# Kernel tuning notes

Hardware: AMD Instinct MI355X
Metric: run time of the kernel (lower is better)

Reference implementation:

```python
import jax, jax.numpy as jnp
import numpy as np

N_NODES = 100000
N_PER_GRAPH = 200
N_GRAPHS = N_NODES // N_PER_GRAPH
N_EDGES = 400000
F_IN = 37
H = 128          # node_hidden == transformer_hidden == fc_hidden
HEADS = 8
K_SEEDS = 75     # ceil(0.25 * 300) -> PyG GMT defaults


def _lin(key, out_d, in_d):
    kw, kb = jax.random.split(key)
    w = jax.random.normal(kw, (out_d, in_d), jnp.float32) * float(1.0 / np.sqrt(in_d))
    b = jax.random.normal(kb, (out_d,), jnp.float32) * 0.02
    return w, b


def gcn_layer(x, W, b, src, dst, n):
    # PyG GCNConv with add_self_loops and symmetric deg^-1/2 normalization
    h = x @ W.T                                   # [n, out]
    deg = jnp.ones((n,), h.dtype).at[dst].add(1.0)   # in-degree + self loop
    dinv = jax.lax.rsqrt(deg)
    msg = h[src] * (dinv[src] * dinv[dst])[:, None]  # gather + edge normalize
    agg = jnp.zeros_like(h).at[dst].add(msg)         # scatter-add
    agg = agg + h * (dinv * dinv)[:, None]           # self-loop message
    return agg + b


def attn_block(Q, K, V, fo_W, fo_b):
    # MAB core of GMT: multi-head attention (scaled by sqrt(dim_V)) + rFF residual
    B, nq, d = Q.shape
    dh = d // HEADS
    Qh = Q.reshape(B, nq, HEADS, dh)
    Kh = K.reshape(B, K.shape[1], HEADS, dh)
    Vh = V.reshape(B, V.shape[1], HEADS, dh)
    scores = jnp.einsum('bqhd,bkhd->bhqk', Qh, Kh) / jnp.sqrt(jnp.asarray(d, Q.dtype))
    A = jax.nn.softmax(scores, axis=-1)
    O = jnp.einsum('bhqk,bkhd->bqhd', A, Vh).reshape(B, nq, d)
    out = Q + O
    return out + jax.nn.relu(out @ fo_W.T + fo_b)


def setup_inputs() -> dict:
    key = jax.random.key(0)
    k = iter(jax.random.split(key, 64))
    inp = {}
    inp['herg_em'] = jax.random.normal(next(k), (1, 1280), jnp.float32)
    inp['x'] = jax.random.normal(next(k), (N_NODES, F_IN), jnp.float32)
    inp['edge_attr'] = jax.random.normal(next(k), (N_EDGES, 4), jnp.float32)
    inp['mol_rep'] = jax.random.normal(next(k), (N_GRAPHS, 11), jnp.float32)
    for i, in_d in enumerate([F_IN, H, H, H]):
        inp[f'conv_W{i}'], inp[f'conv_b{i}'] = _lin(next(k), H, in_d)
    inp['lin1_W'], inp['lin1_b'] = _lin(next(k), H, H)
    inp['lin2_W'], inp['lin2_b'] = _lin(next(k), H, H)
    inp['S1'] = jax.random.normal(next(k), (1, K_SEEDS, H), jnp.float32) * 0.1
    for p in ['pma1', 'sab', 'pma2']:
        for nm in ['fq', 'k', 'v', 'fo']:
            inp[f'{p}_{nm}_W'], inp[f'{p}_{nm}_b'] = _lin(next(k), H, H)
    inp['S2'] = jax.random.normal(next(k), (1, 1, H), jnp.float32) * 0.1
    inp['herg_lin_W'], inp['herg_lin_b'] = _lin(next(k), H, 1280)
    inp['herg_out_W'], inp['herg_out_b'] = _lin(next(k), H, 2 * H)
    inp['fc0_W'], inp['fc0_b'] = _lin(next(k), H, H)
    inp['sig_W'], inp['sig_b'] = _lin(next(k), 1, H)
    inp['edge_index'] = jax.random.randint(next(k), (2, N_EDGES), 0, N_NODES, dtype=jnp.int32)
    inp['batch'] = jnp.arange(N_NODES, dtype=jnp.int32) // N_PER_GRAPH
    return inp


def reference(herg_em, x, edge_attr, mol_rep,
              conv_W0, conv_b0, conv_W1, conv_b1, conv_W2, conv_b2, conv_W3, conv_b3,
              lin1_W, lin1_b, lin2_W, lin2_b,
              S1, pma1_fq_W, pma1_fq_b, pma1_k_W, pma1_k_b, pma1_v_W, pma1_v_b, pma1_fo_W, pma1_fo_b,
              sab_fq_W, sab_fq_b, sab_k_W, sab_k_b, sab_v_W, sab_v_b, sab_fo_W, sab_fo_b,
              S2, pma2_fq_W, pma2_fq_b, pma2_k_W, pma2_k_b, pma2_v_W, pma2_v_b, pma2_fo_W, pma2_fo_b,
              herg_lin_W, herg_lin_b, herg_out_W, herg_out_b,
              fc0_W, fc0_b, sig_W, sig_b,
              edge_index, batch):
    src, dst = edge_index[0], edge_index[1]
    n = x.shape[0]

    # stacked GCNConv + ReLU
    h = jax.nn.relu(gcn_layer(x, conv_W0, conv_b0, src, dst, n))
    for W, b in ((conv_W1, conv_b1), (conv_W2, conv_b2), (conv_W3, conv_b3)):
        h = jax.nn.relu(gcn_layer(h, W, b, src, dst, n))

    # GraphMultisetTransformer: lin1 -> GMPool_G -> SelfAtt -> GMPool_I -> lin2
    hx = h @ lin1_W.T + lin1_b                     # [N, H]
    B = N_GRAPHS

    # GMPool_G: seeds attend to GCNConv-projected keys/values (dense per graph)
    Q = jnp.broadcast_to(S1, (B, K_SEEDS, H)) @ pma1_fq_W.T + pma1_fq_b
    K = gcn_layer(hx, pma1_k_W, pma1_k_b, src, dst, n).reshape(B, N_PER_GRAPH, H)
    V = gcn_layer(hx, pma1_v_W, pma1_v_b, src, dst, n).reshape(B, N_PER_GRAPH, H)
    xb = attn_block(Q, K, V, pma1_fo_W, pma1_fo_b)     # [B, 75, H]

    # SelfAtt (SAB)
    Q = xb @ sab_fq_W.T + sab_fq_b
    K = xb @ sab_k_W.T + sab_k_b
    V = xb @ sab_v_W.T + sab_v_b
    xb = attn_block(Q, K, V, sab_fo_W, sab_fo_b)       # [B, 75, H]

    # GMPool_I: single seed, Linear keys/values
    Q = jnp.broadcast_to(S2, (B, 1, H)) @ pma2_fq_W.T + pma2_fq_b
    K = xb @ pma2_k_W.T + pma2_k_b
    V = xb @ pma2_v_W.T + pma2_v_b
    xb = attn_block(Q, K, V, pma2_fo_W, pma2_fo_b)     # [B, 1, H]

    out = xb[:, 0, :] @ lin2_W.T + lin2_b              # [B, H]

    # hERG branch
    herg = jax.nn.relu(herg_em @ herg_lin_W.T + herg_lin_b)   # [1, 128]
    herg = jnp.broadcast_to(herg, (B, herg.shape[1]))
    out = jnp.concatenate([out, herg], axis=1)                 # [B, 256]
    out = jax.nn.relu(out @ herg_out_W.T + herg_out_b)
    out = jax.nn.relu(out @ fc0_W.T + fc0_b)                   # dropout = identity (eval)
    return jax.nn.sigmoid(out @ sig_W.T + sig_b)               # [B, 1]
```

## Files before the change

### kernel.cpp

```cpp
#include <hip/hip_runtime.h>
#include <hip/hip_bf16.h>

typedef unsigned short ushort_t;
typedef unsigned int uint_t;
typedef __attribute__((ext_vector_type(8))) short short8;
typedef __attribute__((ext_vector_type(4))) float float4v;

static constexpr int NN  = 100000;
static constexpr int NE  = 400000;
static constexpr int NB  = 500;
static constexpr int NS  = 75;
static constexpr int H   = 128;
static constexpr float SCALE = 0.08838834764831845f;

union U32 { uint_t u; float f; };
__device__ __forceinline__ float bf2f(ushort_t b){ U32 t; t.u = ((uint_t)b) << 16; return t.f; }
__device__ __forceinline__ ushort_t f2bf(float f){
    U32 t; t.f = f;
    uint_t r = t.u + 0x7fffu + ((t.u >> 16) & 1u);
    return (ushort_t)(r >> 16);
}
__device__ __forceinline__ void fma8(float* a, uint4 u, float c){
    a[0] += c * bf2f((ushort_t)(u.x & 0xffff)); a[1] += c * bf2f((ushort_t)(u.x >> 16));
    a[2] += c * bf2f((ushort_t)(u.y & 0xffff)); a[3] += c * bf2f((ushort_t)(u.y >> 16));
    a[4] += c * bf2f((ushort_t)(u.z & 0xffff)); a[5] += c * bf2f((ushort_t)(u.z >> 16));
    a[6] += c * bf2f((ushort_t)(u.w & 0xffff)); a[7] += c * bf2f((ushort_t)(u.w >> 16));
}

__global__ void k_hist(int* counts, const int* __restrict__ dst, int e){
    int i = blockIdx.x*256 + threadIdx.x;
    if (i < e) atomicAdd(&counts[dst[i]], 1);
}
__global__ __launch_bounds__(256) void k_scan1(const int* __restrict__ counts,
    int* __restrict__ row_start, int* __restrict__ blockSums,
    float* __restrict__ dinv, float* __restrict__ selfc, int n){
    __shared__ int s[256];
    int t = threadIdx.x, i = blockIdx.x*256 + t;
    int v = (i < n) ? counts[i] : 0;
    s[t] = v; __syncthreads();
    #pragma unroll
    for (int off = 1; off < 256; off <<= 1){
        int add = (t >= off) ? s[t-off] : 0;
        __syncthreads();
        s[t] += add;
        __syncthreads();
    }
    if (i < n){
        row_start[i] = s[t] - v;
        float r = rsqrtf(1.f + (float)v);
        dinv[i] = r; selfc[i] = r*r;
    }
    if (t == 255) blockSums[blockIdx.x] = s[255];
}
__global__ __launch_bounds__(512) void k_scan2(const int* __restrict__ blockSums,
    int* __restrict__ blockOff, int nb){
    __shared__ int s[512];
    int t = threadIdx.x;
    int v = (t < nb) ? blockSums[t] : 0;
    s[t] = v; __syncthreads();
    #pragma unroll
    for (int off = 1; off < 512; off <<= 1){
        int add = (t >= off) ? s[t-off] : 0;
        __syncthreads();
        s[t] += add;
        __syncthreads();
    }
    blockOff[t] = s[t] - v;
}
__global__ void k_scan3(int* __restrict__ row_start, int* __restrict__ cursor,
                        const int* __restrict__ blockOff, int n, int total){
    int i = blockIdx.x*256 + threadIdx.x;
    if (i < n){
        int v = row_start[i] + blockOff[i >> 8];
        row_start[i] = v; cursor[i] = v;
    }
    if (i == 0) row_start[n] = total;
}
__global__ void k_fillcsr(const int* __restrict__ src, const int* __restrict__ dst,
    const float* __restrict__ dinv, int* cursor,
    int* __restrict__ srcs_s, float* __restrict__ ce_s, int e){
    int i = blockIdx.x*256 + threadIdx.x;
    if (i < e){
        int d = dst[i], s = src[i];
        int p = atomicAdd(&cursor[d], 1);
        srcs_s[p] = s;
        ce_s[p] = dinv[s] * dinv[d];
    }
}

struct CvtArgs { const float* w[17]; const float* w0; const float* s1; const float* s2; const float* x37; };
static constexpr int CVT_W   = 17*16384;
static constexpr int CVT_W0  = 8192;
static constexpr int CVT_S1  = 9600;
static constexpr int CVT_S2  = 128;
static constexpr int CVT_X   = NN*64;
__global__ void k_cvt_all(CvtArgs a, ushort_t* __restrict__ wbf, ushort_t* __restrict__ w0bf,
                          ushort_t* __restrict__ s1bf, ushort_t* __restrict__ s2bf,
                          ushort_t* __restrict__ xb64, int* __restrict__ counts){
    int i = blockIdx.x*256 + threadIdx.x;
    if (i < NN) counts[i] = 0;
    if (i < CVT_W){ int idx = i >> 14, off = i & 16383; wbf[i] = f2bf(a.w[idx][off]); return; }
    i -= CVT_W;
    if (i < CVT_W0){ int r = i >> 6, c = i & 63; w0bf[i] = (c < 37) ? f2bf(a.w0[r*37 + c]) : (ushort_t)0; return; }
    i -= CVT_W0;
    if (i < CVT_S1){ s1bf[i] = f2bf(a.s1[i]); return; }
    i -= CVT_S1;
    if (i < CVT_S2){ s2bf[i] = f2bf(a.s2[i]); return; }
    i -= CVT_S2;
    if (i < CVT_X){ int r = i >> 6, c = i & 63; xb64[i] = (c < 37) ? f2bf(a.x37[(size_t)r*37 + c]) : (ushort_t)0; return; }
}

__global__ __launch_bounds__(256) void k_seedq(
    const ushort_t* __restrict__ s1bf, const ushort_t* __restrict__ s2bf,
    const ushort_t* __restrict__ W1, const float* __restrict__ bias1,
    const ushort_t* __restrict__ W2q, const float* __restrict__ bias2,
    ushort_t* __restrict__ q0, ushort_t* __restrict__ q2,
    const float* __restrict__ hem, const float* __restrict__ hlW,
    const float* __restrict__ hlb, float* __restrict__ hergv)
{
    int blk = blockIdx.x;
    int tid  = threadIdx.x;
    if (blk == 3){
        __shared__ float e[1280];
        for (int i = tid; i < 1280; i += 256) e[i] = hem[i];
        __syncthreads();
        if (tid < 128){
            float acc = 0.f;
            for (int k = 0; k < 1280; ++k) acc += e[k] * hlW[(size_t)tid*1280 + k];
            hergv[tid] = fmaxf(acc + hlb[tid], 0.f);
        }
        return;
    }
    const ushort_t* x = (blk < 2) ? s1bf : s2bf;
    const ushort_t* W = (blk < 2) ? W1 : W2q;
    const float* bias = (blk < 2) ? bias1 : bias2;
    ushort_t* out = (blk < 2) ? q0 : q2;
    int M = (blk < 2) ? NS : 1;
    int base = (blk < 2) ? blk*64 : 0;
    int wid  = tid >> 6;
    int lane = tid & 63;
    int l15  = lane & 15, quad = lane >> 4;
    int row0 = base + wid*16;
    int ar   = row0 + l15; if (ar > M-1) ar = M-1;
    const short* xr = (const short*)(x + (size_t)ar*H) + quad*8;
    float4v acc[8];
    #pragma unroll
    for (int i = 0; i < 8; ++i) acc[i] = (float4v)0.f;
    #pragma unroll
    for (int kc = 0; kc < 4; ++kc){
        short8 a = *(const short8*)(xr + kc*32);
        #pragma unroll
        for (int nt = 0; nt < 8; ++nt){
            short8 b = *(const short8*)((const short*)(W + (size_t)(nt*16 + l15)*H) + kc*32 + quad*8);
            acc[nt] = __builtin_amdgcn_mfma_f32_16x16x32_bf16(a, b, acc[nt], 0, 0, 0);
        }
    }
    #pragma unroll
    for (int nt = 0; nt < 8; ++nt){
        int c = nt*16 + l15;
        float bv = bias[c];
        #pragma unroll
        for (int reg = 0; reg < 4; ++reg){
            int r = row0 + quad*4 + reg;
            if (r >= M) continue;
            out[(size_t)r*H + c] = f2bf(acc[nt][reg] + bv);
        }
    }
}

template<int NOUT2>
__global__ __launch_bounds__(256, 4) void gemm_fo_then(
    const ushort_t* __restrict__ x, int M,
    const ushort_t* __restrict__ Wfo, const float* __restrict__ bfo,
    const ushort_t* __restrict__ W2,
    const float* __restrict__ b20, const float* __restrict__ b21, const float* __restrict__ b22,
    ushort_t* __restrict__ o0, ushort_t* __restrict__ o1, ushort_t* __restrict__ o2,
    float* __restrict__ o32)
{
    __shared__ ushort_t As[64][136];
    const int tid = threadIdx.x, w = tid >> 6, lane = tid & 63;
    const int l15 = lane & 15, quad = lane >> 4;
    const int row0 = blockIdx.x*64 + w*16;
    int ar = row0 + l15; if (ar > M-1) ar = M-1;
    const short* xr = (const short*)(x + (size_t)ar*H) + quad*8;
    {
        float4v acc[8];
        #pragma unroll
        for (int i = 0; i < 8; ++i) acc[i] = (float4v)0.f;
        #pragma unroll
        for (int kc = 0; kc < 4; ++kc){
            short8 a = *(const short8*)(xr + kc*32);
            #pragma unroll
            for (int nt = 0; nt < 8; ++nt){
                short8 b = *(const short8*)((const short*)(Wfo + (size_t)(nt*16 + l15)*H) + kc*32 + quad*8);
                acc[nt] = __builtin_amdgcn_mfma_f32_16x16x32_bf16(a, b, acc[nt], 0, 0, 0);
            }
        }
        #pragma unroll
        for (int nt = 0; nt < 8; ++nt){
            int c = nt*16 + l15;
            float bv = bfo[c];
            #pragma unroll
            for (int reg = 0; reg < 4; ++reg){
                int r = row0 + quad*4 + reg;
                float v = 0.f;
                if (r < M) v = fmaxf(acc[nt][reg] + bv, 0.f) + bf2f(x[(size_t)r*H + c]);
                As[w*16 + quad*4 + reg][c] = f2bf(v);
            }
        }
    }
    __syncthreads();
    #pragma unroll 1
    for (int n = 0; n < NOUT2; ++n){
        float4v o[8];
        #pragma unroll
        for (int i = 0; i < 8; ++i) o[i] = (float4v)0.f;
        #pragma unroll
        for (int kc = 0; kc < 4; ++kc){
            short8 a = *(const short8*)(&As[w*16 + l15][kc*32 + quad*8]);
            #pragma unroll
            for (int nt = 0; nt < 8; ++nt){
                short8 b = *(const short8*)((const short*)(W2 + (size_t)((n*8 + nt)*16 + l15)*H) + kc*32 + quad*8);
                o[nt] = __builtin_amdgcn_mfma_f32_16x16x32_bf16(a, b, o[nt], 0, 0, 0);
            }
        }
        ushort_t* out = (n == 0) ? o0 : ((n == 1) ? o1 : o2);
        const float* bb = (n == 0) ? b20 : ((n == 1) ? b21 : b22);
        #pragma unroll
        for (int nt = 0; nt < 8; ++nt){
            int c = nt*16 + l15;
            float bv = bb[c];
            #pragma unroll
            for (int reg = 0; reg < 4; ++reg){
                int r = row0 + quad*4 + reg;
                if (r >= M) continue;
                float v = o[nt][reg] + bv;
                if (o32 && n == 0) o32[(size_t)r*H + c] = v;
                else               out[(size_t)r*H + c] = f2bf(v);
            }
        }
    }
}

template<int NOUT, int RELU, int STAGE2, int MINW>
__global__ __launch_bounds__(256, MINW) void k_conv_fused3(
    const ushort_t* __restrict__ x,
    const int* __restrict__ row_st, const int* __restrict__ srcs,
    const float* __restrict__ ces, const float* __restrict__ selfc,
    const ushort_t* __restrict__ W, const float* __restrict__ bias0,
    const float* __restrict__ bias1,
    const ushort_t* __restrict__ W2, const float* __restrict__ bias2,
    ushort_t* __restrict__ out0, ushort_t* __restrict__ out1)
{
    __shared__ ushort_t As[32][136];
    __shared__ ushort_t Bs[(NOUT==16)?32:1][(NOUT==16)?136:1];
    const int tid = threadIdx.x;
    const int node = tid >> 3, qq = tid & 7;
    const int g = blockIdx.x*32 + node;
    float acc[16];
    #pragma unroll
    for (int i = 0; i < 16; ++i) acc[i] = 0.f;
    if (g < NN){
        const uint4* xr = (const uint4*)(x + (size_t)g*H + qq*16);
        float sc = selfc[g];
        uint4 u0 = xr[0], u1 = xr[1];
        fma8(acc+0, u0, sc); fma8(acc+8, u1, sc);
        int e = row_st[g], e1 = row_st[g+1];
        int sA = 0, sB = 0; float cA = 0.f, cB = 0.f;
        if (e < e1){ sA = srcs[e]; cA = ces[e]; }
        if (e + 1 < e1){ sB = srcs[e+1]; cB = ces[e+1]; }
        while (e + 2 <= e1){
            int sA2 = 0, sB2 = 0; float cA2 = 0.f, cB2 = 0.f;
            if (e + 2 < e1){ sA2 = srcs[e+2]; cA2 = ces[e+2]; }
            if (e + 3 < e1){ sB2 = srcs[e+3]; cB2 = ces[e+3]; }
            const uint4* pa = (const uint4*)(x + (size_t)sA*H + qq*16);
            const uint4* pb = (const uint4*)(x + (size_t)sB*H + qq*16);
            uint4 a0 = pa[0], a1 = pa[1];
            uint4 c0 = pb[0], c1 = pb[1];
            fma8(acc+0, a0, cA); fma8(acc+8, a1, cA);
            fma8(acc+0, c0, cB); fma8(acc+8, c1, cB);
            sA = sA2; sB = sB2; cA = cA2; cB = cB2;
            e += 2;
        }
        if (e < e1){
            const uint4* pa = (const uint4*)(x + (size_t)sA*H + qq*16);
            uint4 a0 = pa[0], a1 = pa[1];
            fma8(acc+0, a0, cA); fma8(acc+8, a1, cA);
        }
    }
    {
        uint_t* dst = (uint_t*)&As[node][qq*16];
        #pragma unroll
        for (int i = 0; i < 8; ++i)
            dst[i] = (uint_t)f2bf(acc[2*i]) | ((uint_t)f2bf(acc[2*i+1]) << 16);
    }
    __syncthreads();
    const int w = tid >> 6, lane = tid & 63, l15 = lane & 15, quad = lane >> 4;
    const int rt = w & 1;
    constexpr int NT = NOUT/2;
    const int ct0 = (w >> 1) * NT;
    float4v o[NT];
    #pragma unroll
    for (int t = 0; t < NT; ++t) o[t] = (float4v)0.f;
    #pragma unroll
    for (int kc = 0; kc < 4; ++kc){
        short8 a = *(const short8*)(&As[rt*16 + l15][kc*32 + quad*8]);
        #pragma unroll
        for (int t = 0; t < NT; ++t){
            short8 bfr = *(const short8*)(W + (size_t)((ct0 + t)*16 + l15)*H + kc*32 + quad*8);
            o[t] = __builtin_amdgcn_mfma_f32_16x16x32_bf16(a, bfr, o[t], 0, 0, 0);
        }
    }
    __syncthreads();
    #pragma unroll
    for (int t = 0; t < NT; ++t){
        int cg = (ct0 + t)*16 + l15;
        #pragma unroll
        for (int r = 0; r < 4; ++r){
            float v;
            if (NOUT == 8 || cg < 128){
                v = o[t][r] + bias0[cg];
                if (RELU) v = fmaxf(v, 0.f);
                As[rt*16 + quad*4 + r][cg] = f2bf(v);
            } else {
                v = o[t][r] + bias1[cg - 128];
                if (RELU) v = fmaxf(v, 0.f);
                Bs[rt*16 + quad*4 + r][cg - 128] = f2bf(v);
            }
        }
    }
    __syncthreads();
    if (STAGE2){
        float4v o2[4];
        #pragma unroll
        for (int t = 0; t < 4; ++t) o2[t] = (float4v)0.f;
        const int ct2 = (w >> 1) * 4;
        #pragma unroll
        for (int kc = 0; kc < 4; ++kc){
            short8 a = *(const short8*)(&As[rt*16 + l15][kc*32 + quad*8]);
            #pragma unroll
            for (int t = 0; t < 4; ++t){
                short8 bfr = *(const short8*)(W2 + (size_t)((ct2 + t)*16 + l15)*H + kc*32 + quad*8);
                o2[t] = __builtin_amdgcn_mfma_f32_16x16x32_bf16(a, bfr, o2[t], 0, 0, 0);
            }
        }
        __syncthreads();
        #pragma unroll
        for (int t = 0; t < 4; ++t){
            int cg = (ct2 + t)*16 + l15;
            #pragma unroll
            for (int r = 0; r < 4; ++r)
                As[rt*16 + quad*4 + r][cg] = f2bf(o2[t][r] + bias2[cg]);
        }
        __syncthreads();
    }
    if (g < NN){
        if (NOUT == 16){
            size_t kb = ((size_t)(qq >> 1)*NN + (size_t)g)*32 + (size_t)(qq & 1)*16;
            ((uint4*)(out0 + kb))[0] = *(const uint4*)&As[node][qq*16];
            ((uint4*)(out0 + kb))[1] = *(const uint4*)&As[node][qq*16 + 8];
            ((uint4*)(out1 + kb))[0] = *(const uint4*)&Bs[node][qq*16];
            ((uint4*)(out1 + kb))[1] = *(const uint4*)&Bs[node][qq*16 + 8];
        } else {
            uint4* op = (uint4*)(out0 + (size_t)g*H + qq*16);
            const uint4* sp = (const uint4*)&As[node][qq*16];
            op[0] = sp[0]; op[1] = sp[1];
        }
    }
}

__global__ __launch_bounds__(256, 8) void k_conv0b(
    const ushort_t* __restrict__ x,
    const int* __restrict__ row_st, const int* __restrict__ srcs,
    const float* __restrict__ ces, const float* __restrict__ selfc,
    const ushort_t* __restrict__ W,
    const float* __restrict__ bias,
    ushort_t* __restrict__ out)
{
    __shared__ ushort_t As[32][136];
    const int tid = threadIdx.x;
    const int node = tid >> 3, qq = tid & 7;
    const int g = blockIdx.x*32 + node;
    float acc[8];
    #pragma unroll
    for (int i = 0; i < 8; ++i) acc[i] = 0.f;
    if (g < NN){
        const uint4* xr = (const uint4*)(x + (size_t)g*64 + qq*8);
        float sc = selfc[g];
        fma8(acc, xr[0], sc);
        int e = row_st[g], e1 = row_st[g+1];
        int sA = 0, sB = 0; float cA = 0.f, cB = 0.f;
        if (e < e1){ sA = srcs[e]; cA = ces[e]; }
        if (e + 1 < e1){ sB = srcs[e+1]; cB = ces[e+1]; }
        while (e + 2 <= e1){
            int sA2 = 0, sB2 = 0; float cA2 = 0.f, cB2 = 0.f;
            if (e + 2 < e1){ sA2 = srcs[e+2]; cA2 = ces[e+2]; }
            if (e + 3 < e1){ sB2 = srcs[e+3]; cB2 = ces[e+3]; }
            uint4 a0 = *(const uint4*)(x + (size_t)sA*64 + qq*8);
            uint4 c0 = *(const uint4*)(x + (size_t)sB*64 + qq*8);
            fma8(acc, a0, cA);
            fma8(acc, c0, cB);
            sA = sA2; sB = sB2; cA = cA2; cB = cB2;
            e += 2;
        }
        if (e < e1){
            uint4 a0 = *(const uint4*)(x + (size_t)sA*64 + qq*8);
            fma8(acc, a0, cA);
        }
    }
    {
        uint_t* dst = (uint_t*)&As[node][qq*8];
        #pragma unroll
        for (int i = 0; i < 4; ++i)
            dst[i] = (uint_t)f2bf(acc[2*i]) | ((uint_t)f2bf(acc[2*i+1]) << 16);
    }
    __syncthreads();
    const int w = tid >> 6, lane = tid & 63, l15 = lane & 15, quad = lane >> 4;
    const int rt = w & 1;
    const int ct0 = (w >> 1) * 4;
    float4v o[4];
    #pragma unroll
    for (int t = 0; t < 4; ++t) o[t] = (float4v)0.f;
    #pragma unroll
    for (int kc = 0; kc < 2; ++kc){
        short8 a = *(const short8*)(&As[rt*16 + l15][kc*32 + quad*8]);
        #pragma unroll
        for (int t = 0; t < 4; ++t){
            short8 bfr = *(const short8*)(W + (size_t)((ct0 + t)*16 + l15)*64 + kc*32 + quad*8);
            o[t] = __builtin_amdgcn_mfma_f32_16x16x32_bf16(a, bfr, o[t], 0, 0, 0);
        }
    }
    __syncthreads();
    #pragma unroll
    for (int t = 0; t < 4; ++t){
        int cg = (ct0 + t)*16 + l15;
        #pragma unroll
        for (int r = 0; r < 4; ++r)
            As[rt*16 + quad*4 + r][cg] = f2bf(fmaxf(o[t][r] + bias[cg], 0.f));
    }
    __syncthreads();
    if (g < NN){
        uint4* op = (uint4*)(out + (size_t)g*H + qq*16);
        const uint4* sp = (const uint4*)&As[node][qq*16];
        op[0] = sp[0]; op[1] = sp[1];
    }
}

template<int NK, int HM>
__global__ __launch_bounds__(256) void k_attn_mfma(
    const ushort_t* __restrict__ Q, int qbs,
    const ushort_t* __restrict__ K, const ushort_t* __restrict__ V,
    ushort_t* __restrict__ out, int nq)
{
    constexpr int NKT = (NK + 15) / 16;
    constexpr int NKC = (NK + 31) / 32;
    __shared__ ushort_t Ks[2][208][24];
    __shared__ ushort_t Vs[2][16][232];
    __shared__ ushort_t Ps[4][16][232];
    int b = blockIdx.x >> 2, hp = blockIdx.x & 3;
    int h0 = hp*2;
    int tid = threadIdx.x;
    {
        uint_t* p = (uint_t*)&Ps[0][0][0];
        for (int i = tid; i < 4*16*232/2; i += 256) p[i] = 0;
    }
    const ushort_t* Kb = HM ? (K + ((size_t)hp*NB + b)*NK*32)
                            : (K + (size_t)b*NK*H + h0*16);
    for (int idx = tid; idx < NK*8; idx += 256){
        int key = idx >> 3, p = idx & 7;
        int hh = p >> 2, dl = (p & 3)*4;
        const uint_t* src = HM ? (const uint_t*)(Kb + (size_t)key*32 + hh*16 + dl)
                               : (const uint_t*)(Kb + (size_t)key*H + hh*16 + dl);
        uint_t* d = (uint_t*)&Ks[hh][key][dl];
        d[0] = src[0]; d[1] = src[1];
    }
    const ushort_t* Vb = HM ? (V + ((size_t)hp*NB + b)*NK*32)
                            : (V + (size_t)b*NK*H + h0*16);
    for (int idx = tid; idx < NK*8; idx += 256){
        int key = idx >> 3, p = idx & 7;
        int hh = p >> 2, dl = (p & 3)*4;
        const ushort_t* src = HM ? (Vb + (size_t)key*32 + hh*16 + dl)
                                 : (Vb + (size_t)key*H + hh*16 + dl);
        Vs[hh][dl+0][key] = src[0];
        Vs[hh][dl+1][key] = src[1];
        Vs[hh][dl+2][key] = src[2];
        Vs[hh][dl+3][key] = src[3];
    }
    for (int idx = tid; idx < 2*16*(232-NK); idx += 256){
        int key = NK + idx % (232-NK), r = idx / (232-NK);
        Vs[r>>4][r&15][key] = 0;
    }
    __syncthreads();

    int w = tid >> 6, lane = tid & 63;
    int hh = w >> 1, half = w & 1;
    int h = h0 + hh;
    int l15 = lane & 15, quad = lane >> 4;
    bool klow = (quad < 2);
    int nqt = (nq + 15) >> 4;
    int split = (nqt + 1) >> 1;
    int qt0 = half ? split : 0;
    int qt1 = half ? nqt : split;
    for (int qt = qt0; qt < qt1; ++qt){
        int qr = qt*16 + l15; if (qr > nq-1) qr = nq-1;
        short8 av = *(const short8*)(Q + (size_t)b*qbs + (size_t)qr*H + h*16 + (quad & 1)*8);
        short8 zero8 = (short8)0;
        short8 afrag = klow ? av : zero8;
        float4v s[NKT];
        #pragma unroll
        for (int kt = 0; kt < NKT; ++kt){
            short8 bv = *(const short8*)(&Ks[hh][kt*16 + l15][(quad & 1)*8]);
            short8 bfrag = klow ? bv : zero8;
            s[kt] = __builtin_amdgcn_mfma_f32_16x16x32_bf16(afrag, bfrag, (float4v)0.f, 0, 0, 0);
        }
        float mx[4] = {-1e30f, -1e30f, -1e30f, -1e30f};
        #pragma unroll
        for (int kt = 0; kt < NKT; ++kt){
            if (kt*16 + l15 >= NK){ s[kt][0]=-1e30f; s[kt][1]=-1e30f; s[kt][2]=-1e30f; s[kt][3]=-1e30f; }
            #pragma unroll
            for (int r = 0; r < 4; ++r) mx[r] = fmaxf(mx[r], s[kt][r]);
        }
        #pragma unroll
        for (int off = 1; off < 16; off <<= 1){
            #pragma unroll
            for (int r = 0; r < 4; ++r) mx[r] = fmaxf(mx[r], __shfl_xor(mx[r], off));
        }
        float sum[4] = {0.f, 0.f, 0.f, 0.f};
        #pragma unroll
        for (int kt = 0; kt < NKT; ++kt){
            #pragma unroll
            for (int r = 0; r < 4; ++r){
                float e = __expf((s[kt][r] - mx[r]) * SCALE);
                sum[r] += e;
                Ps[w][quad*4 + r][kt*16 + l15] = f2bf(e);
            }
        }
        #pragma unroll
        for (int off = 1; off < 16; off <<= 1){
            #pragma unroll
            for (int r = 0; r < 4; ++r) sum[r] += __shfl_xor(sum[r], off);
        }
        float4v o = (float4v)0.f;
        #pragma unroll
        for (int kc = 0; kc < NKC; ++kc){
            short8 pa = *(const short8*)(&Ps[w][l15][kc*32 + quad*8]);
            short8 vb = *(const short8*)(&Vs[hh][l15][kc*32 + quad*8]);
            o = __builtin_amdgcn_mfma_f32_16x16x32_bf16(pa, vb, o, 0, 0, 0);
        }
        #pragma unroll
        for (int r = 0; r < 4; ++r){
            int row = qt*16 + quad*4 + r;
            if (row < nq){
                float qv = bf2f(Q[(size_t)b*qbs + (size_t)row*H + h*16 + l15]);
                out[((size_t)b*nq + row)*H + h*16 + l15] = f2bf(qv + o[r] / sum[r]);
            }
        }
    }
}

__global__ __launch_bounds__(256) void k_pma2_final(
    const ushort_t* __restrict__ q2,
    const ushort_t* __restrict__ K,
    const ushort_t* __restrict__ V,
    const ushort_t* __restrict__ p2foW,
    const float* __restrict__ p2fob,
    const ushort_t* __restrict__ lin2W,
    const float* __restrict__ lin2b,
    const float* __restrict__ hergv,
    const float* __restrict__ hoW, const float* __restrict__ hob,
    const float* __restrict__ fcW, const float* __restrict__ fcb,
    const float* __restrict__ sW,  const float* __restrict__ sb,
    float* __restrict__ outp)
{
    int b = blockIdx.x, t = threadIdx.x;
    __shared__ float sc[8][76];
    __shared__ float sumh[8];
    __shared__ ushort_t xa[128];
    __shared__ ushort_t xb3[128];
    __shared__ float tt[128];
    __shared__ float v256[256];
    __shared__ float red[128];

    const ushort_t* Kb = K + (size_t)b*NS*H;
    const ushort_t* Vb = V + (size_t)b*NS*H;

    {
        int h = t >> 5, l32 = t & 31;
        const ushort_t* qr = q2 + h*16;
        for (int k = l32; k < NS; k += 32){
            const ushort_t* kr = Kb + (size_t)k*H + h*16;
            float s = 0.f;
            #pragma unroll
            for (int d = 0; d < 16; ++d) s += bf2f(qr[d]) * bf2f(kr[d]);
            sc[h][k] = s;
        }
    }
    __syncthreads();
    if (t < 128){
        int hh = t >> 4, i = t & 15;
        float mx = -1e30f;
        for (int k = i; k < NS; k += 16) mx = fmaxf(mx, sc[hh][k]);
        #pragma unroll
        for (int off = 1; off < 16; off <<= 1) mx = fmaxf(mx, __shfl_xor(mx, off));
        float sm = 0.f;
        for (int k = i; k < NS; k += 16){
            float e = __expf((sc[hh][k] - mx) * SCALE);
            sc[hh][k] = e;
            sm += e;
        }
        #pragma unroll
        for (int off = 1; off < 16; off <<= 1) sm += __shfl_xor(sm, off);
        if (i == 0) sumh[hh] = sm;
    }
    __syncthreads();
    if (t < 128){
        int hh = t >> 4;
        float o = 0.f;
        for (int k = 0; k < NS; ++k) o += sc[hh][k] * bf2f(Vb[(size_t)k*H + t]);
        xa[t] = f2bf(bf2f(q2[t]) + o / sumh[hh]);
    }
    __syncthreads();
    if (t < 128){
        float a = 0.f;
        const ushort_t* wr = p2foW + (size_t)t*H;
        for (int k = 0; k < H; ++k) a += bf2f(xa[k]) * bf2f(wr[k]);
        xb3[t] = f2bf(fmaxf(a + p2fob[t], 0.f) + bf2f(xa[t]));
    }
    __syncthreads();
    if (t < 128){
        float a = 0.f;
        const ushort_t* wr = lin2W + (size_t)t*H;
        for (int k = 0; k < H; ++k) a += bf2f(xb3[k]) * bf2f(wr[k]);
        v256[t] = a + lin2b[t];
        v256[128 + t] = hergv[t];
    }
    __syncthreads();
    if (t < 128){
        float acc = 0.f;
        const float* wr = hoW + (size_t)t*256;
        for (int k = 0; k < 256; ++k) acc += v256[k] * wr[k];
        tt[t] = fmaxf(acc + hob[t], 0.f);
    }
    __syncthreads();
    if (t < 128){
        float acc = 0.f;
        const float* wr = fcW + (size_t)t*128;
        for (int k = 0; k < 128; ++k) acc += tt[k] * wr[k];
        float uv = fmaxf(acc + fcb[t], 0.f);
        red[t] = uv * sW[t];
    }
    __syncthreads();
    for (int s = 64; s > 0; s >>= 1){
        if (t < s) red[t] += red[t + s];
        __syncthreads();
    }
    if (t == 0){
        float logit = red[0] + sb[0];
        outp[b] = 1.f / (1.f + expf(-logit));
    }
}

extern "C" void kernel_launch(void* const* d_in, const int* in_sizes, int n_in,
                              void* d_out, int out_size, void* d_ws, size_t ws_size,
                              hipStream_t stream)
{
    (void)in_sizes; (void)n_in; (void)out_size; (void)ws_size;
    const float* herg_em = (const float*)d_in[0];
    const float* x_in    = (const float*)d_in[1];
    const float* convW[4] = {(const float*)d_in[4], (const float*)d_in[6], (const float*)d_in[8], (const float*)d_in[10]};
    const float* convB[4] = {(const float*)d_in[5], (const float*)d_in[7], (const float*)d_in[9], (const float*)d_in[11]};
    const float* lin1W = (const float*)d_in[12]; const float* lin1b = (const float*)d_in[13];
    const float* lin2W = (const float*)d_in[14]; const float* lin2b = (const float*)d_in[15];
    const float* S1    = (const float*)d_in[16];
    const float* p1fqW = (const float*)d_in[17]; const float* p1fqb = (const float*)d_in[18];
    const float* p1kW  = (const float*)d_in[19]; const float* p1kb  = (const float*)d_in[20];
    const float* p1vW  = (const float*)d_in[21]; const float* p1vb  = (const float*)d_in[22];
    const float* p1foW = (const float*)d_in[23]; const float* p1fob = (const float*)d_in[24];
    const float* sfqW  = (const float*)d_in[25]; const float* sfqb  = (const float*)d_in[26];
    const float* skW   = (const float*)d_in[27]; const float* skb   = (const float*)d_in[28];
    const float* svW   = (const float*)d_in[29]; const float* svb   = (const float*)d_in[30];
    const float* sfoW  = (const float*)d_in[31]; const float* sfob  = (const float*)d_in[32];
    const float* p2fqW = (const float*)d_in[33]; const float* p2fqb = (const float*)d_in[34];
    const float* p2kW  = (const float*)d_in[35]; const float* p2kb  = (const float*)d_in[36];
    const float* p2vW  = (const float*)d_in[37]; const float* p2vb  = (const float*)d_in[38];
    const float* p2foW = (const float*)d_in[39]; const float* p2fob = (const float*)d_in[40];
    const float* S2    = (const float*)d_in[41];
    const float* hlW   = (const float*)d_in[42]; const float* hlb   = (const float*)d_in[43];
    const float* hoW   = (const float*)d_in[44]; const float* hob   = (const float*)d_in[45];
    const float* fcW   = (const float*)d_in[46]; const float* fcb   = (const float*)d_in[47];
    const float* sW    = (const float*)d_in[48]; const float* sb    = (const float*)d_in[49];
    const int*  ei    = (const int*)d_in[50];
    const int*  esrc  = ei;
    const int*  edst  = ei + NE;
    float* outp = (float*)d_out;

    char* WS = (char*)d_ws;
    int*   counts = (int*)(WS + 0);
    int*   cursor = (int*)(WS + 400384);
    int*   row_st = (int*)(WS + 800768);
    int*   bSums  = (int*)(WS + 1201152);
    int*   bOff   = (int*)(WS + 1203200);
    float* dinv   = (float*)(WS + 1205248);
    float* selfc  = (float*)(WS + 1605632);
    int*   srcs_s = (int*)(WS + 2005632);
    float* ce_s   = (float*)(WS + 3605632);
    ushort_t* wbf = (ushort_t*)(WS + 5205632);
    ushort_t* w0bf= (ushort_t*)(WS + 5762688);
    ushort_t* s1bf= (ushort_t*)(WS + 5779072);
    ushort_t* s2bf= (ushort_t*)(WS + 5798272);
    ushort_t* q0  = (ushort_t*)(WS + 5798528);
    ushort_t* q2  = (ushort_t*)(WS + 5817728);
    float* hergv  = (float*)(WS + 5817984);
    ushort_t* xb64= (ushort_t*)(WS + 6074496);
    ushort_t* b0  = (ushort_t*)(WS + 18874496);
    ushort_t* b1  = (ushort_t*)(WS + 44474496);
    ushort_t* b2  = (ushort_t*)(WS + 70074496);
    ushort_t* xA  = (ushort_t*)(WS + 95674496);
    ushort_t* xB  = (ushort_t*)(WS + 105275520);
    ushort_t* xQ  = (ushort_t*)(WS + 114876544);
    ushort_t* xK  = (ushort_t*)(WS + 124477568);
    ushort_t* xV  = (ushort_t*)(WS + 134078592);

    const int gN   = (NN + 255)/256;
    const int gE   = (NE + 255)/256;
    const int gC   = (NN + 31)/32;
    const int gXb  = (NB*NS + 63)/64;

    CvtArgs ca;
    ca.w[0]=convW[1]; ca.w[1]=convW[2]; ca.w[2]=convW[3]; ca.w[3]=lin1W; ca.w[4]=lin2W;
    ca.w[5]=p1kW; ca.w[6]=p1vW; ca.w[7]=p1foW;
    ca.w[8]=sfqW; ca.w[9]=skW; ca.w[10]=svW; ca.w[11]=sfoW;
    ca.w[12]=p2kW; ca.w[13]=p2vW; ca.w[14]=p2foW; ca.w[15]=p1fqW; ca.w[16]=p2fqW;
    ca.w0 = convW[0]; ca.s1 = S1; ca.s2 = S2; ca.x37 = x_in;
    const int cvtTotal = CVT_W + CVT_W0 + CVT_S1 + CVT_S2 + CVT_X;
    k_cvt_all<<<(cvtTotal + 255)/256, 256, 0, stream>>>(ca, wbf, w0bf, s1bf, s2bf, xb64, counts);

    k_hist  <<<gE, 256, 0, stream>>>(counts, edst, NE);
    k_scan1 <<<gN, 256, 0, stream>>>(counts, row_st, bSums, dinv, selfc, NN);
    k_scan2 <<<1, 512, 0, stream>>>(bSums, bOff, gN);
    k_scan3 <<<gN, 256, 0, stream>>>(row_st, cursor, bOff, NN, NE);
    k_fillcsr<<<gE, 256, 0, stream>>>(esrc, edst, dinv, cursor, srcs_s, ce_s, NE);

    k_seedq<<<4, 256, 0, stream>>>(s1bf, s2bf, wbf + (size_t)15*16384, p1fqb,
                                   wbf + (size_t)16*16384, p2fqb, q0, q2,
                                   herg_em, hlW, hlb, hergv);

    k_conv0b<<<gC, 256, 0, stream>>>(xb64, row_st, srcs_s, ce_s, selfc, w0bf, convB[0], b0);
    k_conv_fused3<8,1,0,8><<<gC, 256, 0, stream>>>(b0, row_st, srcs_s, ce_s, selfc,
        wbf + (size_t)0*16384, convB[1], nullptr, nullptr, nullptr, b1, nullptr);
    k_conv_fused3<8,1,0,8><<<gC, 256, 0, stream>>>(b1, row_st, srcs_s, ce_s, selfc,
        wbf + (size_t)1*16384, convB[2], nullptr, nullptr, nullptr, b0, nullptr);
    k_conv_fused3<8,1,1,8><<<gC, 256, 0, stream>>>(b0, row_st, srcs_s, ce_s, selfc,
        wbf + (size_t)2*16384, convB[3], nullptr, wbf + (size_t)3*16384, lin1b, b1, nullptr);
    k_conv_fused3<16,0,0,4><<<gC, 256, 0, stream>>>(b1, row_st, srcs_s, ce_s, selfc,
        wbf + (size_t)5*16384, p1kb, p1vb, nullptr, nullptr, b2, b0);
    k_attn_mfma<200,1><<<NB*4, 256, 0, stream>>>(q0, 0, b2, b0, xA, NS);
    gemm_fo_then<3><<<gXb, 256, 0, stream>>>(xA, NB*NS, wbf + (size_t)7*16384, p1fob,
        wbf + (size_t)8*16384, sfqb, skb, svb, xQ, xK, xV, nullptr);
    k_attn_mfma<75,0><<<NB*4, 256, 0, stream>>>(xQ, NS*H, xK, xV, xB, NS);
    gemm_fo_then<2><<<gXb, 256, 0, stream>>>(xB, NB*NS, wbf + (size_t)11*16384, sfob,
        wbf + (size_t)12*16384, p2kb, p2vb, nullptr, xK, xV, nullptr, nullptr);
    k_pma2_final<<<NB, 256, 0, stream>>>(q2, xK, xV,
        wbf + (size_t)14*16384, p2fob, wbf + (size_t)4*16384, lin2b,
        hergv, hoW, hob, fcW, fcb, sW, sb, outp);
}
```

Baseline: 771.9 us.

## Fuse post-PMA1 tail into one per-graph kernel kept in shared memory

Replaces the two gemm_fo_then launches, the SAB attention launch and the final PMA2 kernel with one kernel, one block per graph. All intermediate Q/K/V and activations for a graph's 75 seeds stay in LDS instead of round-tripping through global memory. The intent is to remove roughly 4 launches and several tens of MB of intermediate traffic. In exchange it uses large LDS per block, so at most one or two blocks fit per CU, and there are only 500 blocks, which may leave the GPU underutilized and serialize the GEMM work within each block.

Measured after the change: 731.7 us. -5.2%, faster.

```diff
diff --git a/kernel.cpp b/kernel.cpp
--- a/kernel.cpp
+++ b/kernel.cpp
@@ -164,80 +164,6 @@
             int r = row0 + quad*4 + reg;
             if (r >= M) continue;
             out[(size_t)r*H + c] = f2bf(acc[nt][reg] + bv);
-        }
-    }
-}
-
-template<int NOUT2>
-__global__ __launch_bounds__(256, 4) void gemm_fo_then(
-    const ushort_t* __restrict__ x, int M,
-    const ushort_t* __restrict__ Wfo, const float* __restrict__ bfo,
-    const ushort_t* __restrict__ W2,
-    const float* __restrict__ b20, const float* __restrict__ b21, const float* __restrict__ b22,
-    ushort_t* __restrict__ o0, ushort_t* __restrict__ o1, ushort_t* __restrict__ o2,
-    float* __restrict__ o32)
-{
-    __shared__ ushort_t As[64][136];
-    const int tid = threadIdx.x, w = tid >> 6, lane = tid & 63;
-    const int l15 = lane & 15, quad = lane >> 4;
-    const int row0 = blockIdx.x*64 + w*16;
-    int ar = row0 + l15; if (ar > M-1) ar = M-1;
-    const short* xr = (const short*)(x + (size_t)ar*H) + quad*8;
-    {
-        float4v acc[8];
-        #pragma unroll
-        for (int i = 0; i < 8; ++i) acc[i] = (float4v)0.f;
-        #pragma unroll
-        for (int kc = 0; kc < 4; ++kc){
-            short8 a = *(const short8*)(xr + kc*32);
-            #pragma unroll
-            for (int nt = 0; nt < 8; ++nt){
-                short8 b = *(const short8*)((const short*)(Wfo + (size_t)(nt*16 + l15)*H) + kc*32 + quad*8);
-                acc[nt] = __builtin_amdgcn_mfma_f32_16x16x32_bf16(a, b, acc[nt], 0, 0, 0);
-            }
-        }
-        #pragma unroll
-        for (int nt = 0; nt < 8; ++nt){
-            int c = nt*16 + l15;
-            float bv = bfo[c];
-            #pragma unroll
-            for (int reg = 0; reg < 4; ++reg){
-                int r = row0 + quad*4 + reg;
-                float v = 0.f;
-                if (r < M) v = fmaxf(acc[nt][reg] + bv, 0.f) + bf2f(x[(size_t)r*H + c]);
-                As[w*16 + quad*4 + reg][c] = f2bf(v);
-            }
-        }
-    }
-    __syncthreads();
-    #pragma unroll 1
-    for (int n = 0; n < NOUT2; ++n){
-        float4v o[8];
-        #pragma unroll
-        for (int i = 0; i < 8; ++i) o[i] = (float4v)0.f;
-        #pragma unroll
-        for (int kc = 0; kc < 4; ++kc){
-            short8 a = *(const short8*)(&As[w*16 + l15][kc*32 + quad*8]);
-            #pragma unroll
-            for (int nt = 0; nt < 8; ++nt){
-                short8 b = *(const short8*)((const short*)(W2 + (size_t)((n*8 + nt)*16 + l15)*H) + kc*32 + quad*8);
-                o[nt] = __builtin_amdgcn_mfma_f32_16x16x32_bf16(a, b, o[nt], 0, 0, 0);
-            }
-        }
-        ushort_t* out = (n == 0) ? o0 : ((n == 1) ? o1 : o2);
-        const float* bb = (n == 0) ? b20 : ((n == 1) ? b21 : b22);
-        #pragma unroll
-        for (int nt = 0; nt < 8; ++nt){
-            int c = nt*16 + l15;
-            float bv = bb[c];
-            #pragma unroll
-            for (int reg = 0; reg < 4; ++reg){
-                int r = row0 + quad*4 + reg;
-                if (r >= M) continue;
-                float v = o[nt][reg] + bv;
-                if (o32 && n == 0) o32[(size_t)r*H + c] = v;
-                else               out[(size_t)r*H + c] = f2bf(v);
-            }
         }
     }
 }
@@ -558,105 +484,301 @@
     }
 }
 
-__global__ __launch_bounds__(256) void k_pma2_final(
-    const ushort_t* __restrict__ q2,
-    const ushort_t* __restrict__ K,
-    const ushort_t* __restrict__ V,
-    const ushort_t* __restrict__ p2foW,
-    const float* __restrict__ p2fob,
-    const ushort_t* __restrict__ lin2W,
-    const float* __restrict__ lin2b,
-    const float* __restrict__ hergv,
-    const float* __restrict__ hoW, const float* __restrict__ hob,
-    const float* __restrict__ fcW, const float* __restrict__ fcb,
-    const float* __restrict__ sW,  const float* __restrict__ sb,
-    float* __restrict__ outp)
-{
-    int b = blockIdx.x, t = threadIdx.x;
-    __shared__ float sc[8][76];
-    __shared__ float sumh[8];
-    __shared__ ushort_t xa[128];
-    __shared__ ushort_t xb3[128];
-    __shared__ float tt[128];
-    __shared__ float v256[256];
-    __shared__ float red[128];
-
-    const ushort_t* Kb = K + (size_t)b*NS*H;
-    const ushort_t* Vb = V + (size_t)b*NS*H;
-
+struct TailArgs {
+    const ushort_t* xA; const ushort_t* q2;
+    const ushort_t* p1foW; const float* p1fob;
+    const ushort_t* sfqW;  const float* sfqb;
+    const ushort_t* skW;   const float* skb;
+    const ushort_t* svW;   const float* svb;
+    const ushort_t* sfoW;  const float* sfob;
+    const ushort_t* p2kW;  const float* p2kb;
+    const ushort_t* p2vW;  const float* p2vb;
+    const ushort_t* p2foW; const float* p2fob;
+    const ushort_t* lin2W; const float* lin2b;
+    const float* hergv;
+    const float* hoW; const float* hob;
+    const float* fcW; const float* fcb;
+    const float* sW;  const float* sb;
+    float* outp;
+};
+
+__global__ __launch_bounds__(256, 1) void k_graph_tail(TailArgs a){
+    __shared__ ushort_t bufQ[80*136];
+    __shared__ ushort_t bufX[80*136];
+    __shared__ ushort_t bufK[80*136];
+    __shared__ ushort_t vt[8*16*104];
+    __shared__ ushort_t ps[4*16*104];
+    const int b = blockIdx.x, tid = threadIdx.x;
+    const int w = tid >> 6, lane = tid & 63, l15 = lane & 15, quad = lane >> 4;
+
+    for (int i = tid; i < 8*16*104/2; i += 256) ((uint_t*)vt)[i] = 0u;
+    for (int i = tid; i < 4*16*104/2; i += 256) ((uint_t*)ps)[i] = 0u;
     {
-        int h = t >> 5, l32 = t & 31;
-        const ushort_t* qr = q2 + h*16;
-        for (int k = l32; k < NS; k += 32){
-            const ushort_t* kr = Kb + (size_t)k*H + h*16;
-            float s = 0.f;
+        const ushort_t* xg = a.xA + (size_t)b*NS*H;
+        for (int i = tid; i < NS*16; i += 256){
+            int row = i >> 4, q = i & 15;
+            *(uint4*)(bufQ + row*136 + q*8) = *(const uint4*)(xg + (size_t)row*H + q*8);
+        }
+    }
+    __syncthreads();
+
+    for (int job = w; job < 40; job += 4){
+        int rt = job >> 3, ct = job & 7;
+        float4v o = (float4v)0.f;
+        #pragma unroll
+        for (int kc = 0; kc < 4; ++kc){
+            short8 av = *(const short8*)(bufQ + (rt*16 + l15)*136 + kc*32 + quad*8);
+            short8 bv = *(const short8*)((const short*)(a.p1foW + (size_t)(ct*16 + l15)*H) + kc*32 + quad*8);
+            o = __builtin_amdgcn_mfma_f32_16x16x32_bf16(av, bv, o, 0, 0, 0);
+        }
+        int c = ct*16 + l15; float bb = a.p1fob[c];
+        #pragma unroll
+        for (int r = 0; r < 4; ++r){
+            int row = rt*16 + quad*4 + r;
+            bufX[row*136 + c] = f2bf(fmaxf(o[r] + bb, 0.f) + bf2f(bufQ[row*136 + c]));
+        }
+    }
+    __syncthreads();
+
+    for (int job = w; job < 40; job += 4){
+        int rt = job >> 3, ct = job & 7;
+        float4v o = (float4v)0.f;
+        #pragma unroll
+        for (int kc = 0; kc < 4; ++kc){
+            short8 av = *(const short8*)(bufX + (rt*16 + l15)*136 + kc*32 + quad*8);
+            short8 bv = *(const short8*)((const short*)(a.sfqW + (size_t)(ct*16 + l15)*H) + kc*32 + quad*8);
+            o = __builtin_amdgcn_mfma_f32_16x16x32_bf16(av, bv, o, 0, 0, 0);
+        }
+        int c = ct*16 + l15; float bb = a.sfqb[c];
+        #pragma unroll
+        for (int r = 0; r < 4; ++r)
+            bufQ[(rt*16 + quad*4 + r)*136 + c] = f2bf(o[r] + bb);
+    }
+    for (int job = w; job < 40; job += 4){
+        int rt = job >> 3, ct = job & 7;
+        float4v o = (float4v)0.f;
+        #pragma unroll
+        for (int kc = 0; kc < 4; ++kc){
+            short8 av = *(const short8*)(bufX + (rt*16 + l15)*136 + kc*32 + quad*8);
+            short8 bv = *(const short8*)((const short*)(a.skW + (size_t)(ct*16 + l15)*H) + kc*32 + quad*8);
+            o = __builtin_amdgcn_mfma_f32_16x16x32_bf16(av, bv, o, 0, 0, 0);
+        }
+        int c = ct*16 + l15; float bb = a.skb[c];
+        #pragma unroll
+        for (int r = 0; r < 4; ++r)
+            bufK[(rt*16 + quad*4 + r)*136 + c] = f2bf(o[r] + bb);
+    }
+    for (int job = w; job < 40; job += 4){
+        int rt = job >> 3, ct = job & 7;
+        float4v o = (float4v)0.f;
+        #pragma unroll
+        for (int kc = 0; kc < 4; ++kc){
+            short8 av = *(const short8*)(bufX + (rt*16 + l15)*136 + kc*32 + quad*8);
+            short8 bv = *(const short8*)((const short*)(a.svW + (size_t)(ct*16 + l15)*H) + kc*32 + quad*8);
+            o = __builtin_amdgcn_mfma_f32_16x16x32_bf16(av, bv, o, 0, 0, 0);
+        }
+        int c = ct*16 + l15; float bb = a.svb[c];
+        #pragma unroll
+        for (int r = 0; r < 4; ++r){
+            int key = rt*16 + quad*4 + r;
+            if (key < NS) vt[c*104 + key] = f2bf(o[r] + bb);
+        }
+    }
+    __syncthreads();
+
+    {
+        short8 zero8 = (short8)0;
+        bool klow = (quad < 2);
+        for (int hh = 0; hh < 2; ++hh){
+            int h = w*2 + hh;
+            for (int qt = 0; qt < 5; ++qt){
+                short8 av = *(const short8*)(bufQ + (qt*16 + l15)*136 + h*16 + (quad & 1)*8);
+                short8 afrag = klow ? av : zero8;
+                float4v s[5];
+                #pragma unroll
+                for (int kt = 0; kt < 5; ++kt){
+                    short8 bv = *(const short8*)(bufK + (kt*16 + l15)*136 + h*16 + (quad & 1)*8);
+                    short8 bfrag = klow ? bv : zero8;
+                    s[kt] = __builtin_amdgcn_mfma_f32_16x16x32_bf16(afrag, bfrag, (float4v)0.f, 0, 0, 0);
+                }
+                float mx[4] = {-1e30f, -1e30f, -1e30f, -1e30f};
+                #pragma unroll
+                for (int kt = 0; kt < 5; ++kt){
+                    if (kt*16 + l15 >= NS){ s[kt][0]=-1e30f; s[kt][1]=-1e30f; s[kt][2]=-1e30f; s[kt][3]=-1e30f; }
+                    #pragma unroll
+                    for (int r = 0; r < 4; ++r) mx[r] = fmaxf(mx[r], s[kt][r]);
+                }
+                #pragma unroll
+                for (int off = 1; off < 16; off <<= 1){
+                    #pragma unroll
+                    for (int r = 0; r < 4; ++r) mx[r] = fmaxf(mx[r], __shfl_xor(mx[r], off));
+                }
+                float sum[4] = {0.f, 0.f, 0.f, 0.f};
+                #pragma unroll
+                for (int kt = 0; kt < 5; ++kt){
+                    #pragma unroll
+                    for (int r = 0; r < 4; ++r){
+                        float e = __expf((s[kt][r] - mx[r]) * SCALE);
+                        sum[r] += e;
+                        ps[w*1664 + (quad*4 + r)*104 + kt*16 + l15] = f2bf(e);
+                    }
+                }
+                #pragma unroll
+                for (int off = 1; off < 16; off <<= 1){
+                    #pragma unroll
+                    for (int r = 0; r < 4; ++r) sum[r] += __shfl_xor(sum[r], off);
+                }
+                float4v o = (float4v)0.f;
+                #pragma unroll
+                for (int kc = 0; kc < 3; ++kc){
+                    short8 pa = *(const short8*)(ps + w*1664 + l15*104 + kc*32 + quad*8);
+                    short8 vb = *(const short8*)(vt + (h*16 + l15)*104 + kc*32 + quad*8);
+                    o = __builtin_amdgcn_mfma_f32_16x16x32_bf16(pa, vb, o, 0, 0, 0);
+                }
+                #pragma unroll
+                for (int r = 0; r < 4; ++r){
+                    int row = qt*16 + quad*4 + r;
+                    if (row < NS){
+                        float qv = bf2f(bufQ[row*136 + h*16 + l15]);
+                        bufQ[row*136 + h*16 + l15] = f2bf(qv + o[r] / sum[r]);
+                    }
+                }
+            }
+        }
+    }
+    __syncthreads();
+
+    for (int job = w; job < 40; job += 4){
+        int rt = job >> 3, ct = job & 7;
+        float4v o = (float4v)0.f;
+        #pragma unroll
+        for (int kc = 0; kc < 4; ++kc){
+            short8 av = *(const short8*)(bufQ + (rt*16 + l15)*136 + kc*32 + quad*8);
+            short8 bv = *(const short8*)((const short*)(a.sfoW + (size_t)(ct*16 + l15)*H) + kc*32 + quad*8);
+            o = __builtin_amdgcn_mfma_f32_16x16x32_bf16(av, bv, o, 0, 0, 0);
+        }
+        int c = ct*16 + l15; float bb = a.sfob[c];
+        #pragma unroll
+        for (int r = 0; r < 4; ++r){
+            int row = rt*16 + quad*4 + r;
+            bufX[row*136 + c] = f2bf(fmaxf(o[r] + bb, 0.f) + bf2f(bufQ[row*136 + c]));
+        }
+    }
+    __syncthreads();
+
+    for (int job = w; job < 40; job += 4){
+        int rt = job >> 3, ct = job & 7;
+        float4v o = (float4v)0.f;
+        #pragma unroll
+        for (int kc = 0; kc < 4; ++kc){
+            short8 av = *(const short8*)(bufX + (rt*16 + l15)*136 + kc*32 + quad*8);
+            short8 bv = *(const short8*)((const short*)(a.p2kW + (size_t)(ct*16 + l15)*H) + kc*32 + quad*8);
+            o = __builtin_amdgcn_mfma_f32_16x16x32_bf16(av, bv, o, 0, 0, 0);
+        }
+        int c = ct*16 + l15; float bb = a.p2kb[c];
+        #pragma unroll
+        for (int r = 0; r < 4; ++r)
+            bufK[(rt*16 + quad*4 + r)*136 + c] = f2bf(o[r] + bb);
+    }
+    for (int job = w; job < 40; job += 4){
+        int rt = job >> 3, ct = job & 7;
+        float4v o = (float4v)0.f;
+        #pragma unroll
+        for (int kc = 0; kc < 4; ++kc){
+            short8 av = *(const short8*)(bufX + (rt*16 + l15)*136 + kc*32 + quad*8);
+            short8 bv = *(const short8*)((const short*)(a.p2vW + (size_t)(ct*16 + l15)*H) + kc*32 + quad*8);
+            o = __builtin_amdgcn_mfma_f32_16x16x32_bf16(av, bv, o, 0, 0, 0);
+        }
+        int c = ct*16 + l15; float bb = a.p2vb[c];
+        #pragma unroll
+        for (int r = 0; r < 4; ++r)
+            bufQ[(rt*16 + quad*4 + r)*136 + c] = f2bf(o[r] + bb);
+    }
+    __syncthreads();
+
+    {
+        int t = tid;
+        char* sb8 = (char*)ps;
+        float* sc       = (float*)sb8;
+        float* sumh     = (float*)(sb8 + 2432);
+        ushort_t* xa    = (ushort_t*)(sb8 + 2464);
+        ushort_t* xb3   = (ushort_t*)(sb8 + 2720);
+        float* tt       = (float*)(sb8 + 2976);
+        float* v256     = (float*)(sb8 + 3488);
+        float* red      = (float*)(sb8 + 4512);
+        {
+            int h = t >> 5, l32 = t & 31;
+            const ushort_t* qr = a.q2 + h*16;
+            for (int k = l32; k < NS; k += 32){
+                float s = 0.f;
+                #pragma unroll
+                for (int d = 0; d < 16; ++d) s += bf2f(qr[d]) * bf2f(bufK[k*136 + h*16 + d]);
+                sc[h*76 + k] = s;
+            }
+        }
+        __syncthreads();
+        if (t < 128){
+            int hh = t >> 4, i = t & 15;
+            float mx = -1e30f;
+            for (int k = i; k < NS; k += 16) mx = fmaxf(mx, sc[hh*76 + k]);
             #pragma unroll
-            for (int d = 0; d < 16; ++d) s += bf2f(qr[d]) * bf2f(kr[d]);
-            sc[h][k] = s;
-        }
-    }
-    __syncthreads();
-    if (t < 128){
-        int hh = t >> 4, i = t & 15;
-        float mx = -1e30f;
-        for (int k = i; k < NS; k += 16) mx = fmaxf(mx, sc[hh][k]);
-        #pragma unroll
-        for (int off = 1; off < 16; off <<= 1) mx = fmaxf(mx, __shfl_xor(mx, off));
-        float sm = 0.f;
-        for (int k = i; k < NS; k += 16){
-            float e = __expf((sc[hh][k] - mx) * SCALE);
-            sc[hh][k] = e;
-            sm += e;
-        }
-        #pragma unroll
-        for (int off = 1; off < 16; off <<= 1) sm += __shfl_xor(sm, off);
-        if (i == 0) sumh[hh] = sm;
-    }
-    __syncthreads();
-    if (t < 128){
-        int hh = t >> 4;
-        float o = 0.f;
-        for (int k = 0; k < NS; ++k) o += sc[hh][k] * bf2f(Vb[(size_t)k*H + t]);
-        xa[t] = f2bf(bf2f(q2[t]) + o / sumh[hh]);
-    }
-    __syncthreads();
-    if (t < 128){
-        float a = 0.f;
-        const ushort_t* wr = p2foW + (size_t)t*H;
-        for (int k = 0; k < H; ++k) a += bf2f(xa[k]) * bf2f(wr[k]);
-        xb3[t] = f2bf(fmaxf(a + p2fob[t], 0.f) + bf2f(xa[t]));
-    }
-    __syncthreads();
-    if (t < 128){
-        float a = 0.f;
-        const ushort_t* wr = lin2W + (size_t)t*H;
-        for (int k = 0; k < H; ++k) a += bf2f(xb3[k]) * bf2f(wr[k]);
-        v256[t] = a + lin2b[t];
-        v256[128 + t] = hergv[t];
-    }
-    __syncthreads();
-    if (t < 128){
-        float acc = 0.f;
-        const float* wr = hoW + (size_t)t*256;
-        for (int k = 0; k < 256; ++k) acc += v256[k] * wr[k];
-        tt[t] = fmaxf(acc + hob[t], 0.f);
-    }
-    __syncthreads();
-    if (t < 128){
-        float acc = 0.f;
-        const float* wr = fcW + (size_t)t*128;
-        for (int k = 0; k < 128; ++k) acc += tt[k] * wr[k];
-        float uv = fmaxf(acc + fcb[t], 0.f);
-        red[t] = uv * sW[t];
-    }
-    __syncthreads();
-    for (int s = 64; s > 0; s >>= 1){
-        if (t < s) red[t] += red[t + s];
-        __syncthreads();
-    }
-    if (t == 0){
-        float logit = red[0] + sb[0];
-        outp[b] = 1.f / (1.f + expf(-logit));
+            for (int off = 1; off < 16; off <<= 1) mx = fmaxf(mx, __shfl_xor(mx, off));
+            float sm = 0.f;
+            for (int k = i; k < NS; k += 16){
+                float e = __expf((sc[hh*76 + k] - mx) * SCALE);
+                sc[hh*76 + k] = e;
+                sm += e;
+            }
+            #pragma unroll
+            for (int off = 1; off < 16; off <<= 1) sm += __shfl_xor(sm, off);
+            if (i == 0) sumh[hh] = sm;
+        }
+        __syncthreads();
+        if (t < 128){
+            int hh = t >> 4;
+            float o = 0.f;
+            for (int k = 0; k < NS; ++k) o += sc[hh*76 + k] * bf2f(bufQ[k*136 + t]);
+            xa[t] = f2bf(bf2f(a.q2[t]) + o / sumh[hh]);
+        }
+        __syncthreads();
+        if (t < 128){
+            float acc = 0.f;
+            const ushort_t* wr = a.p2foW + (size_t)t*H;
+            for (int k = 0; k < H; ++k) acc += bf2f(xa[k]) * bf2f(wr[k]);
+            xb3[t] = f2bf(fmaxf(acc + a.p2fob[t], 0.f) + bf2f(xa[t]));
+        }
+        __syncthreads();
+        if (t < 128){
+            float acc = 0.f;
+            const ushort_t* wr = a.lin2W + (size_t)t*H;
+            for (int k = 0; k < H; ++k) acc += bf2f(xb3[k]) * bf2f(wr[k]);
+            v256[t] = acc + a.lin2b[t];
+            v256[128 + t] = a.hergv[t];
+        }
+        __syncthreads();
+        if (t < 128){
+            float acc = 0.f;
+            const float* wr = a.hoW + (size_t)t*256;
+            for (int k = 0; k < 256; ++k) acc += v256[k] * wr[k];
+            tt[t] = fmaxf(acc + a.hob[t], 0.f);
+        }
+        __syncthreads();
+        if (t < 128){
+            float acc = 0.f;
+            const float* wr = a.fcW + (size_t)t*128;
+            for (int k = 0; k < 128; ++k) acc += tt[k] * wr[k];
+            float uv = fmaxf(acc + a.fcb[t], 0.f);
+            red[t] = uv * a.sW[t];
+        }
+        __syncthreads();
+        for (int s = 64; s > 0; s >>= 1){
+            if (t < s) red[t] += red[t + s];
+            __syncthreads();
+        }
+        if (t == 0){
+            float logit = red[0] + a.sb[0];
+            a.outp[b] = 1.f / (1.f + expf(-logit));
+        }
     }
 }
 
@@ -716,15 +838,10 @@
     ushort_t* b1  = (ushort_t*)(WS + 44474496);
     ushort_t* b2  = (ushort_t*)(WS + 70074496);
     ushort_t* xA  = (ushort_t*)(WS + 95674496);
-    ushort_t* xB  = (ushort_t*)(WS + 105275520);
-    ushort_t* xQ  = (ushort_t*)(WS + 114876544);
-    ushort_t* xK  = (ushort_t*)(WS + 124477568);
-    ushort_t* xV  = (ushort_t*)(WS + 134078592);
 
     const int gN   = (NN + 255)/256;
     const int gE   = (NE + 255)/256;
     const int gC   = (NN + 31)/32;
-    const int gXb  = (NB*NS + 63)/64;
 
     CvtArgs ca;
     ca.w[0]=convW[1]; ca.w[1]=convW[2]; ca.w[2]=convW[3]; ca.w[3]=lin1W; ca.w[4]=lin2W;
@@ -755,12 +872,22 @@
     k_conv_fused3<16,0,0,4><<<gC, 256, 0, stream>>>(b1, row_st, srcs_s, ce_s, selfc,
         wbf + (size_t)5*16384, p1kb, p1vb, nullptr, nullptr, b2, b0);
     k_attn_mfma<200,1><<<NB*4, 256, 0, stream>>>(q0, 0, b2, b0, xA, NS);
-    gemm_fo_then<3><<<gXb, 256, 0, stream>>>(xA, NB*NS, wbf + (size_t)7*16384, p1fob,
-        wbf + (size_t)8*16384, sfqb, skb, svb, xQ, xK, xV, nullptr);
-    k_attn_mfma<75,0><<<NB*4, 256, 0, stream>>>(xQ, NS*H, xK, xV, xB, NS);
-    gemm_fo_then<2><<<gXb, 256, 0, stream>>>(xB, NB*NS, wbf + (size_t)11*16384, sfob,
-        wbf + (size_t)12*16384, p2kb, p2vb, nullptr, xK, xV, nullptr, nullptr);
-    k_pma2_final<<<NB, 256, 0, stream>>>(q2, xK, xV,
-        wbf + (size_t)14*16384, p2fob, wbf + (size_t)4*16384, lin2b,
-        hergv, hoW, hob, fcW, fcb, sW, sb, outp);
-}
+
+    TailArgs ta;
+    ta.xA = xA; ta.q2 = q2;
+    ta.p1foW = wbf + (size_t)7*16384;  ta.p1fob = p1fob;
+    ta.sfqW  = wbf + (size_t)8*16384;  ta.sfqb  = sfqb;
+    ta.skW   = wbf + (size_t)9*16384;  ta.skb   = skb;
+    ta.svW   = wbf + (size_t)10*16384; ta.svb   = svb;
+    ta.sfoW  = wbf + (size_t)11*16384; ta.sfob  = sfob;
+    ta.p2kW  = wbf + (size_t)12*16384; ta.p2kb  = p2kb;
+    ta.p2vW  = wbf + (size_t)13*16384; ta.p2vb  = p2vb;
+    ta.p2foW = wbf + (size_t)14*16384; ta.p2fob = p2fob;
+    ta.lin2W = wbf + (size_t)4*16384;  ta.lin2b = lin2b;
+    ta.hergv = hergv;
+    ta.hoW = hoW; ta.hob = hob;
+    ta.fcW = fcW; ta.fcb = fcb;
+    ta.sW = sW; ta.sb = sb;
+    ta.outp = outp;
+    k_graph_tail<<<NB, 256, 0, stream>>>(ta);
+}
```
